# Kernel tuning notes

Measured on AMD Instinct MI355X. Metric: run time of the kernel, lower is better.

The kernel has to match this reference:

```python
import jax, jax.numpy as jnp
import numpy as np

N = 50000      # nodes per graph batch (per siamese side)
E = 500000     # edges per side
F_IN = 128     # input_channels
H = 128        # hidden_channels
OUT = 2        # output_channels
G = 512        # number of graphs in the batch


def setup_inputs() -> dict:
    key = jax.random.key(0)
    ks = jax.random.split(key, 16)

    def lin_w(k, fan_in, shape):
        lim = 1.0 / np.sqrt(fan_in)
        return jax.random.uniform(k, shape, jnp.float32, -lim, lim)

    return {
        "x1": jax.random.normal(ks[0], (N, F_IN), jnp.float32),
        "x2": jax.random.normal(ks[1], (N, F_IN), jnp.float32),
        "edge_index1": jax.random.randint(ks[2], (2, E), 0, N, jnp.int32),
        "edge_index2": jax.random.randint(ks[3], (2, E), 0, N, jnp.int32),
        "batch1": jnp.sort(jax.random.randint(ks[4], (N,), 0, G, jnp.int32)),
        "batch2": jnp.sort(jax.random.randint(ks[5], (N,), 0, G, jnp.int32)),
        "W1": lin_w(ks[6], F_IN, (F_IN, H)), "b1": jnp.zeros((H,), jnp.float32),
        "W2": lin_w(ks[7], H, (H, H)),       "b2": jnp.zeros((H,), jnp.float32),
        "W3": lin_w(ks[8], H, (H, H)),       "b3": jnp.zeros((H,), jnp.float32),
        "Wc1": lin_w(ks[9], 2 * H, (2 * H, 4 * H)), "bc1": jnp.zeros((4 * H,), jnp.float32),
        "Wc2": lin_w(ks[10], 4 * H, (4 * H, 2 * H)), "bc2": jnp.zeros((2 * H,), jnp.float32),
        "Wc3": lin_w(ks[11], 2 * H, (2 * H, OUT)),   "bc3": jnp.zeros((OUT,), jnp.float32),
        "num_graphs": G,
    }


def _gcn_layer(x, W, b, src, dst, dinv):
    # PyG GCNConv: linear transform, then deg^{-1/2} A_hat deg^{-1/2} aggregation + bias
    h = x @ W
    msg = h[src] * (dinv[src] * dinv[dst])[:, None]   # [E+N, H]
    return jax.ops.segment_sum(msg, dst, num_segments=x.shape[0]) + b


def _forward_once(x, edge_index, batch, W1, b1, W2, b2, W3, b3, num_graphs):
    n = x.shape[0]
    loop = jnp.arange(n, dtype=edge_index.dtype)
    src = jnp.concatenate([edge_index[0], loop])      # add self-loops
    dst = jnp.concatenate([edge_index[1], loop])
    deg = jax.ops.segment_sum(jnp.ones_like(dst, dtype=x.dtype), dst, num_segments=n)
    dinv = jax.lax.rsqrt(deg)                          # deg >= 1 due to self-loops
    h = jax.nn.relu(_gcn_layer(x, W1, b1, src, dst, dinv))
    h = jax.nn.relu(_gcn_layer(h, W2, b2, src, dst, dinv))
    h = _gcn_layer(h, W3, b3, src, dst, dinv)
    # global_mean_pool over batch indices
    s = jax.ops.segment_sum(h, batch, num_segments=num_graphs)
    cnt = jax.ops.segment_sum(jnp.ones((n,), x.dtype), batch, num_segments=num_graphs)
    return s / jnp.maximum(cnt, 1.0)[:, None]


def reference(x1, x2, edge_index1, edge_index2, batch1, batch2,
              W1, b1, W2, b2, W3, b3, Wc1, bc1, Wc2, bc2, Wc3, bc3, num_graphs):
    g1 = _forward_once(x1, edge_index1, batch1, W1, b1, W2, b2, W3, b3, num_graphs)
    g2 = _forward_once(x2, edge_index2, batch2, W1, b1, W2, b2, W3, b3, num_graphs)
    z = jnp.concatenate([g1, g2], axis=1)             # [G, 2H]
    z = jax.nn.relu(z @ Wc1 + bc1)
    z = jax.nn.relu(z @ Wc2 + bc2)
    # dropout p=0.5 is identity at eval time
    return z @ Wc3 + bc3                               # [G, OUT]
```

## Files before the change

### kernel.cpp

```cpp
#include <hip/hip_runtime.h>
#include <math.h>

#define N_NODES 50000
#define E_EDGES 500000
#define HDIM    128
#define OUTC    2
#define NGRAPH  512

typedef _Float16 f16x8 __attribute__((ext_vector_type(8)));
typedef float    f32x4 __attribute__((ext_vector_type(4)));

__global__ void k_zero(int* __restrict__ p, int n) {
    int i = blockIdx.x * blockDim.x + threadIdx.x;
    int stride = gridDim.x * blockDim.x;
    for (; i < n; i += stride) p[i] = 0;
}

__global__ void k_hist(const int* __restrict__ d0, const int* __restrict__ d1,
                       int ecnt, int off1, int* __restrict__ cnt) {
    int i = blockIdx.x * blockDim.x + threadIdx.x;
    int stride = gridDim.x * blockDim.x;
    for (; i < ecnt; i += stride) {
        int d = (i < E_EDGES) ? d0[i] : d1[i - E_EDGES] + off1;
        atomicAdd(&cnt[d], 1);
    }
}

__global__ void k_scan_a(const int* __restrict__ cnt, int* __restrict__ excl,
                         int* __restrict__ blksum, float* __restrict__ dinv,
                         const int* __restrict__ bt0, const int* __restrict__ bt1,
                         int goff0, int nn, int nside, float* __restrict__ cnt_g) {
    __shared__ int s[512];
    int t = threadIdx.x;
    int i = blockIdx.x * 512 + t;
    int v = 0;
    if (i < nn) {
        v = cnt[i];
        dinv[i] = 1.0f / sqrtf((float)(v + 1));
        int g = (i < nside) ? bt0[i] + goff0 : bt1[i - nside] + NGRAPH;
        atomicAdd(&cnt_g[g], 1.0f);
    }
    s[t] = v; __syncthreads();
    for (int off = 1; off < 512; off <<= 1) {
        int add = (t >= off) ? s[t - off] : 0;
        __syncthreads();
        s[t] += add;
        __syncthreads();
    }
    if (i < nn) excl[i] = s[t] - v;
    if (t == 511) blksum[blockIdx.x] = s[511];
}

__global__ void k_scan_b(int* __restrict__ blksum, int nb) {
    __shared__ int s[512];
    int t = threadIdx.x;
    int v = (t < nb) ? blksum[t] : 0;
    s[t] = v; __syncthreads();
    for (int off = 1; off < 512; off <<= 1) {
        int add = (t >= off) ? s[t - off] : 0;
        __syncthreads();
        s[t] += add;
        __syncthreads();
    }
    if (t < nb) blksum[t] = s[t] - v;
}

__global__ void k_scan_c(int* __restrict__ excl, const int* __restrict__ blksum,
                         int nn, int tot) {
    int t = threadIdx.x;
    int i = blockIdx.x * 512 + t;
    if (i < nn) excl[i] += blksum[blockIdx.x];
    if (i == 0) excl[nn] = tot;
}

__global__ void k_fill(const int* __restrict__ s0, const int* __restrict__ s1,
                       const int* __restrict__ d0, const int* __restrict__ d1,
                       int ecnt, int off1,
                       const int* __restrict__ row_ptr, int* __restrict__ fill_cnt,
                       const float* __restrict__ dinv, int2* __restrict__ edges) {
    int i = blockIdx.x * blockDim.x + threadIdx.x;
    int stride = gridDim.x * blockDim.x;
    for (; i < ecnt; i += stride) {
        int d, sg;
        if (i < E_EDGES) { sg = s0[i]; d = d0[i]; }
        else             { sg = s1[i - E_EDGES] + off1; d = d1[i - E_EDGES] + off1; }
        int p = atomicAdd(&fill_cnt[d], 1);
        float w = dinv[sg] * dinv[d];
        edges[row_ptr[d] + p] = make_int2(sg, __float_as_int(w));
    }
}

__global__ void k_cvt(const float* __restrict__ x0, const float* __restrict__ x1,
                      int nside_pairs, int total_pairs,
                      _Float16* __restrict__ hi, _Float16* __restrict__ lo) {
    int i = blockIdx.x * blockDim.x + threadIdx.x;
    int stride = gridDim.x * blockDim.x;
    for (; i < total_pairs; i += stride) {
        float2 v = (i < nside_pairs) ? ((const float2*)x0)[i]
                                     : ((const float2*)x1)[i - nside_pairs];
        _Float16 hx = (_Float16)v.x, hy = (_Float16)v.y;
        _Float16 lx = (_Float16)(v.x - (float)hx), ly = (_Float16)(v.y - (float)hy);
        union { _Float16 h[2]; unsigned u; } ph, pl;
        ph.h[0] = hx; ph.h[1] = hy;
        pl.h[0] = lx; pl.h[1] = ly;
        ((unsigned*)hi)[i] = ph.u;
        ((unsigned*)lo)[i] = pl.u;
    }
}

__global__ void k_cvtw(const float* __restrict__ W,
                       _Float16* __restrict__ thi, _Float16* __restrict__ tlo) {
    int i = blockIdx.x * blockDim.x + threadIdx.x;
    if (i >= 128 * 128) return;
    int n = i >> 7, k = i & 127;
    float v = W[k * 128 + n];
    _Float16 h = (_Float16)v;
    thi[i] = h;
    tlo[i] = (_Float16)(v - (float)h);
}

__global__ __launch_bounds__(256) void k_gemm_splitf16(
        const _Float16* __restrict__ Ahi, const _Float16* __restrict__ Alo,
        const _Float16* __restrict__ Bhi, const _Float16* __restrict__ Blo,
        float* __restrict__ C, int M) {
    __shared__ _Float16 sA[2][128][40];
    __shared__ _Float16 sB[2][128][40];
    int tid = threadIdx.x;
    int wave = tid >> 6, lane = tid & 63;
    int wm = (wave >> 1) * 64;
    int wn = (wave & 1) * 64;
    int quad = lane >> 4, fm = lane & 15;
    int row0 = blockIdx.x * 128;

    int lr = tid >> 2;
    int lk = (tid & 3) * 8;

    f32x4 acc[4][4] = {};

    const float4 z4 = make_float4(0.f, 0.f, 0.f, 0.f);
    for (int kc = 0; kc < 128; kc += 32) {
        int r1 = row0 + lr, r2 = row0 + lr + 64;
        bool ok1 = r1 < M, ok2 = r2 < M;
        float4 ah1 = ok1 ? *(const float4*)(Ahi + (size_t)r1 * 128 + kc + lk) : z4;
        float4 al1 = ok1 ? *(const float4*)(Alo + (size_t)r1 * 128 + kc + lk) : z4;
        float4 ah2 = ok2 ? *(const float4*)(Ahi + (size_t)r2 * 128 + kc + lk) : z4;
        float4 al2 = ok2 ? *(const float4*)(Alo + (size_t)r2 * 128 + kc + lk) : z4;
        float4 bh1 = *(const float4*)(Bhi + (size_t)lr * 128 + kc + lk);
        float4 bl1 = *(const float4*)(Blo + (size_t)lr * 128 + kc + lk);
        float4 bh2 = *(const float4*)(Bhi + (size_t)(lr + 64) * 128 + kc + lk);
        float4 bl2 = *(const float4*)(Blo + (size_t)(lr + 64) * 128 + kc + lk);
        __syncthreads();
        *(float4*)&sA[0][lr][lk]      = ah1;
        *(float4*)&sA[1][lr][lk]      = al1;
        *(float4*)&sA[0][lr + 64][lk] = ah2;
        *(float4*)&sA[1][lr + 64][lk] = al2;
        *(float4*)&sB[0][lr][lk]      = bh1;
        *(float4*)&sB[1][lr][lk]      = bl1;
        *(float4*)&sB[0][lr + 64][lk] = bh2;
        *(float4*)&sB[1][lr + 64][lk] = bl2;
        __syncthreads();

        f16x8 afh[4], afl[4], bfh[4], bfl[4];
#pragma unroll
        for (int mi = 0; mi < 4; mi++) {
            afh[mi] = *(const f16x8*)&sA[0][wm + mi * 16 + fm][quad * 8];
            afl[mi] = *(const f16x8*)&sA[1][wm + mi * 16 + fm][quad * 8];
        }
#pragma unroll
        for (int ni = 0; ni < 4; ni++) {
            bfh[ni] = *(const f16x8*)&sB[0][wn + ni * 16 + fm][quad * 8];
            bfl[ni] = *(const f16x8*)&sB[1][wn + ni * 16 + fm][quad * 8];
        }
#pragma unroll
        for (int mi = 0; mi < 4; mi++)
#pragma unroll
            for (int ni = 0; ni < 4; ni++) {
                acc[mi][ni] = __builtin_amdgcn_mfma_f32_16x16x32_f16(afh[mi], bfh[ni], acc[mi][ni], 0, 0, 0);
                acc[mi][ni] = __builtin_amdgcn_mfma_f32_16x16x32_f16(afh[mi], bfl[ni], acc[mi][ni], 0, 0, 0);
                acc[mi][ni] = __builtin_amdgcn_mfma_f32_16x16x32_f16(afl[mi], bfh[ni], acc[mi][ni], 0, 0, 0);
            }
    }

#pragma unroll
    for (int mi = 0; mi < 4; mi++)
#pragma unroll
        for (int reg = 0; reg < 4; reg++) {
            int r = row0 + wm + mi * 16 + quad * 4 + reg;
            if (r >= M) continue;
#pragma unroll
            for (int ni = 0; ni < 4; ni++)
                C[(size_t)r * 128 + wn + ni * 16 + fm] = acc[mi][ni][reg];
        }
}

__global__ __launch_bounds__(256) void k_gemm(
        const float* __restrict__ A, const float* __restrict__ B,
        const float* __restrict__ bias, float* __restrict__ C,
        int M, int Nn, int K, int ldc, int act) {
    __shared__ float As[16][64];
    __shared__ float Bs[16][68];
    int tid = threadIdx.x;
    int tx = tid & 15, ty = tid >> 4;
    int row0 = blockIdx.x * 64, col0 = blockIdx.y * 64;
    float acc[4][4] = {};
    int arow = tid >> 2;
    int acol = (tid & 3) * 4;
    int brow = tid >> 4;
    int bcol = (tid & 15) * 4;

    for (int k0 = 0; k0 < K; k0 += 16) {
        float4 av = make_float4(0.f, 0.f, 0.f, 0.f);
        int ar = row0 + arow;
        if (ar < M) av = *(const float4*)(A + (size_t)ar * K + k0 + acol);
        As[acol + 0][arow] = av.x;
        As[acol + 1][arow] = av.y;
        As[acol + 2][arow] = av.z;
        As[acol + 3][arow] = av.w;

        float4 bv = make_float4(0.f, 0.f, 0.f, 0.f);
        const float* Brow = B + (size_t)(k0 + brow) * Nn;
        int bc = col0 + bcol;
        if (bc + 3 < Nn) {
            bv = *(const float4*)(Brow + bc);
        } else {
            if (bc     < Nn) bv.x = Brow[bc];
            if (bc + 1 < Nn) bv.y = Brow[bc + 1];
            if (bc + 2 < Nn) bv.z = Brow[bc + 2];
        }
        Bs[brow][bcol + 0] = bv.x;
        Bs[brow][bcol + 1] = bv.y;
        Bs[brow][bcol + 2] = bv.z;
        Bs[brow][bcol + 3] = bv.w;
        __syncthreads();

#pragma unroll
        for (int k = 0; k < 16; k++) {
            float4 a = *(const float4*)&As[k][ty * 4];
            float4 b = *(const float4*)&Bs[k][tx * 4];
            acc[0][0] += a.x * b.x; acc[0][1] += a.x * b.y; acc[0][2] += a.x * b.z; acc[0][3] += a.x * b.w;
            acc[1][0] += a.y * b.x; acc[1][1] += a.y * b.y; acc[1][2] += a.y * b.z; acc[1][3] += a.y * b.w;
            acc[2][0] += a.z * b.x; acc[2][1] += a.z * b.y; acc[2][2] += a.z * b.z; acc[2][3] += a.z * b.w;
            acc[3][0] += a.w * b.x; acc[3][1] += a.w * b.y; acc[3][2] += a.w * b.z; acc[3][3] += a.w * b.w;
        }
        __syncthreads();
    }

#pragma unroll
    for (int i = 0; i < 4; i++) {
        int r = row0 + ty * 4 + i;
        if (r >= M) continue;
#pragma unroll
        for (int j = 0; j < 4; j++) {
            int c = col0 + tx * 4 + j;
            if (c >= Nn) continue;
            float v = acc[i][j];
            if (bias) v += bias[c];
            if (act) v = fmaxf(v, 0.0f);
            C[(size_t)r * ldc + c] = v;
        }
    }
}

template <int MODE, int PACK>
__global__ __launch_bounds__(256) void k_agg(
        const float* __restrict__ H, const float* __restrict__ dinv,
        const int* __restrict__ row_ptr, const int2* __restrict__ edges,
        const float* __restrict__ bias,
        _Float16* __restrict__ outHi, _Float16* __restrict__ outLo,
        float* __restrict__ outF,
        const int* __restrict__ bt0, const int* __restrict__ bt1,
        int goff0, int nnodes, int nside, float* __restrict__ pool) {
    int wave = threadIdx.x >> 6, lane = threadIdx.x & 63;
    int node = blockIdx.x * 4 + wave;
    if (node >= nnodes) return;

    float di = dinv[node];
    float2 hv = ((const float2*)(H + (size_t)node * HDIM))[lane];
    float wself = di * di;
    float ax = hv.x * wself;
    float ay = hv.y * wself;

    int rs = __builtin_amdgcn_readfirstlane(row_ptr[node]);
    int re = __builtin_amdgcn_readfirstlane(row_ptr[node + 1]);
    for (int base = rs; base < re; base += 8) {
        int nrem = re - base;
        int m = nrem - 1;
        int i1 = 1 < nrem ? 1 : m;
        int i2 = 2 < nrem ? 2 : m;
        int i3 = 3 < nrem ? 3 : m;
        int i4 = 4 < nrem ? 4 : m;
        int i5 = 5 < nrem ? 5 : m;
        int i6 = 6 < nrem ? 6 : m;
        int i7 = 7 < nrem ? 7 : m;
        int2 E0 = edges[base];
        int2 E1 = edges[base + i1];
        int2 E2 = edges[base + i2];
        int2 E3 = edges[base + i3];
        int2 E4 = edges[base + i4];
        int2 E5 = edges[base + i5];
        int2 E6 = edges[base + i6];
        int2 E7 = edges[base + i7];
        float2 v0 = ((const float2*)(H + (size_t)E0.x * HDIM))[lane];
        float2 v1 = ((const float2*)(H + (size_t)E1.x * HDIM))[lane];
        float2 v2 = ((const float2*)(H + (size_t)E2.x * HDIM))[lane];
        float2 v3 = ((const float2*)(H + (size_t)E3.x * HDIM))[lane];
        float2 v4 = ((const float2*)(H + (size_t)E4.x * HDIM))[lane];
        float2 v5 = ((const float2*)(H + (size_t)E5.x * HDIM))[lane];
        float2 v6 = ((const float2*)(H + (size_t)E6.x * HDIM))[lane];
        float2 v7 = ((const float2*)(H + (size_t)E7.x * HDIM))[lane];
        float w0 = __int_as_float(E0.y);
        float w1 = 1 < nrem ? __int_as_float(E1.y) : 0.f;
        float w2 = 2 < nrem ? __int_as_float(E2.y) : 0.f;
        float w3 = 3 < nrem ? __int_as_float(E3.y) : 0.f;
        float w4 = 4 < nrem ? __int_as_float(E4.y) : 0.f;
        float w5 = 5 < nrem ? __int_as_float(E5.y) : 0.f;
        float w6 = 6 < nrem ? __int_as_float(E6.y) : 0.f;
        float w7 = 7 < nrem ? __int_as_float(E7.y) : 0.f;
        ax = fmaf(v0.x, w0, ax); ay = fmaf(v0.y, w0, ay);
        ax = fmaf(v1.x, w1, ax); ay = fmaf(v1.y, w1, ay);
        ax = fmaf(v2.x, w2, ax); ay = fmaf(v2.y, w2, ay);
        ax = fmaf(v3.x, w3, ax); ay = fmaf(v3.y, w3, ay);
        ax = fmaf(v4.x, w4, ax); ay = fmaf(v4.y, w4, ay);
        ax = fmaf(v5.x, w5, ax); ay = fmaf(v5.y, w5, ay);
        ax = fmaf(v6.x, w6, ax); ay = fmaf(v6.y, w6, ay);
        ax = fmaf(v7.x, w7, ax); ay = fmaf(v7.y, w7, ay);
    }

    if (MODE == 2) {
        int g = (node < nside) ? bt0[node] + goff0 : bt1[node - nside] + NGRAPH;
        float* p = pool + (size_t)g * HDIM + lane * 2;
        atomicAdd(p,     ax);
        atomicAdd(p + 1, ay);
    } else {
        float ox = fmaxf(ax + bias[lane * 2],     0.0f);
        float oy = fmaxf(ay + bias[lane * 2 + 1], 0.0f);
        if (PACK) {
            _Float16 hx = (_Float16)ox, hy = (_Float16)oy;
            _Float16 lx = (_Float16)(ox - (float)hx), ly = (_Float16)(oy - (float)hy);
            union { _Float16 h[2]; unsigned u; } ph, pl;
            ph.h[0] = hx; ph.h[1] = hy;
            pl.h[0] = lx; pl.h[1] = ly;
            ((unsigned*)(outHi + (size_t)node * HDIM))[lane] = ph.u;
            ((unsigned*)(outLo + (size_t)node * HDIM))[lane] = pl.u;
        } else {
            ((float2*)(outF + (size_t)node * HDIM))[lane] = make_float2(ox, oy);
        }
    }
}

__global__ void k_divpool(float* __restrict__ pool, const float* __restrict__ cnt_g) {
    int i = blockIdx.x * blockDim.x + threadIdx.x;
    if (i < 2 * NGRAPH * HDIM) pool[i] /= fmaxf(cnt_g[i >> 7], 1.0f);
}

extern "C" void kernel_launch(void* const* d_in, const int* in_sizes, int n_in,
                              void* d_out, int out_size, void* d_ws, size_t ws_size,
                              hipStream_t stream) {
    (void)in_sizes; (void)n_in; (void)out_size;

    const float* x[2]  = {(const float*)d_in[0], (const float*)d_in[1]};
    const int*   ei[2] = {(const int*)d_in[2], (const int*)d_in[3]};
    const int*   bt[2] = {(const int*)d_in[4], (const int*)d_in[5]};
    const float* W1  = (const float*)d_in[6];  const float* b1  = (const float*)d_in[7];
    const float* W2  = (const float*)d_in[8];  const float* b2  = (const float*)d_in[9];
    const float* W3  = (const float*)d_in[10]; const float* b3  = (const float*)d_in[11];
    const float* Wc1 = (const float*)d_in[12]; const float* bc1 = (const float*)d_in[13];
    const float* Wc2 = (const float*)d_in[14]; const float* bc2 = (const float*)d_in[15];
    const float* Wc3 = (const float*)d_in[16]; const float* bc3 = (const float*)d_in[17];
    float* out = (float*)d_out;

    const bool batched = ws_size >= 120ull * 1000 * 1000;
    const int NN = batched ? 2 * N_NODES : N_NODES;
    const int NE = batched ? 2 * E_EDGES : E_EDGES;

    char* ws = (char*)d_ws;
    size_t off = 0;
    auto carve = [&](size_t bytes) -> char* {
        char* p = ws + off;
        off += (bytes + 255) & ~(size_t)255;
        return p;
    };

    int*   edge_cnt = (int*)  carve((size_t)NN * 4);
    int*   fill_cnt = (int*)  carve((size_t)NN * 4);
    float* pool_s   = (float*)carve((size_t)2 * NGRAPH * HDIM * 4);
    float* cnt_g    = (float*)carve((size_t)2 * NGRAPH * 4);
    float* dinv     = (float*)carve((size_t)NN * 4);
    int*   row_ptr  = (int*)  carve((size_t)(NN + 1) * 4);
    int2*  edges    = (int2*) carve((size_t)NE * 8);
    int*   blksum   = (int*)  carve(1024 * 4);
    _Float16* wt    = (_Float16*)carve(4 * 128 * 128 * 2);
    _Float16* hS    = (_Float16*)carve((size_t)NN * HDIM * 4);
    float* hA       = (float*)carve((size_t)NN * HDIM * 4);
    float* zcat     = (float*)carve((size_t)NGRAPH * 2 * HDIM * 4);
    float* z1       = (float*)carve((size_t)NGRAPH * 4 * HDIM * 4);
    float* z2       = (float*)carve((size_t)NGRAPH * 2 * HDIM * 4);

    _Float16* w1hi = wt;
    _Float16* w1lo = wt + 128 * 128;
    _Float16* w2hi = wt + 2 * 128 * 128;
    _Float16* w2lo = wt + 3 * 128 * 128;
    _Float16* hShi = hS;
    _Float16* hSlo = hS + (size_t)NN * HDIM;
    float*    hSf  = (float*)hS;

    int zeroA_words = (int)(((char*)pool_s - (char*)edge_cnt) / 4);
    int zeroB_words = (int)(((char*)dinv   - (char*)pool_s)   / 4);

    k_zero<<<256, 256, 0, stream>>>((int*)pool_s, zeroB_words);
    k_cvtw<<<64, 256, 0, stream>>>(W1, w1hi, w1lo);
    k_cvtw<<<64, 256, 0, stream>>>(W2, w2hi, w2lo);

    const int gblk = (NN + 127) / 128;

    if (batched) {
        const int nscan = (2 * N_NODES + 511) / 512;
        const int ablk  = (2 * N_NODES + 3) / 4;

        k_zero<<<512, 256, 0, stream>>>(edge_cnt, zeroA_words);
        k_hist<<<1024, 256, 0, stream>>>(ei[0] + E_EDGES, ei[1] + E_EDGES,
                                         2 * E_EDGES, N_NODES, edge_cnt);
        k_scan_a<<<nscan, 512, 0, stream>>>(edge_cnt, row_ptr, blksum, dinv,
                                            bt[0], bt[1], 0, 2 * N_NODES, N_NODES, cnt_g);
        k_scan_b<<<1, 512, 0, stream>>>(blksum, nscan);
        k_scan_c<<<nscan, 512, 0, stream>>>(row_ptr, blksum, 2 * N_NODES, 2 * E_EDGES);
        k_fill<<<1024, 256, 0, stream>>>(ei[0], ei[1], ei[0] + E_EDGES, ei[1] + E_EDGES,
                                         2 * E_EDGES, N_NODES, row_ptr, fill_cnt, dinv, edges);

        k_cvt<<<1024, 256, 0, stream>>>(x[0], x[1], N_NODES * HDIM / 2,
                                        2 * N_NODES * HDIM / 2, hShi, hSlo);

        k_gemm_splitf16<<<gblk, 256, 0, stream>>>(hShi, hSlo, w1hi, w1lo, hA, 2 * N_NODES);
        k_agg<0, 1><<<ablk, 256, 0, stream>>>(hA, dinv, row_ptr, edges, b1,
                                              hShi, hSlo, nullptr, bt[0], bt[1], 0,
                                              2 * N_NODES, N_NODES, nullptr);
        k_gemm_splitf16<<<gblk, 256, 0, stream>>>(hShi, hSlo, w2hi, w2lo, hA, 2 * N_NODES);
        k_agg<0, 0><<<ablk, 256, 0, stream>>>(hA, dinv, row_ptr, edges, b2,
                                              nullptr, nullptr, hSf, bt[0], bt[1], 0,
                                              2 * N_NODES, N_NODES, nullptr);
        k_agg<2, 0><<<ablk, 256, 0, stream>>>(hSf, dinv, row_ptr, edges, nullptr,
                                              nullptr, nullptr, nullptr, bt[0], bt[1], 0,
                                              2 * N_NODES, N_NODES, pool_s);
    } else {
        const int nscan = (N_NODES + 511) / 512;
        const int ablk  = (N_NODES + 3) / 4;

        for (int s = 0; s < 2; ++s) {
            const int* esrc = ei[s];
            const int* edst = ei[s] + E_EDGES;
            int goff = s * NGRAPH;

            k_zero<<<512, 256, 0, stream>>>(edge_cnt, zeroA_words);
            k_hist<<<512, 256, 0, stream>>>(edst, edst, E_EDGES, 0, edge_cnt);
            k_scan_a<<<nscan, 512, 0, stream>>>(edge_cnt, row_ptr, blksum, dinv,
                                                bt[s], bt[s], goff, N_NODES, N_NODES, cnt_g);
            k_scan_b<<<1, 512, 0, stream>>>(blksum, nscan);
            k_scan_c<<<nscan, 512, 0, stream>>>(row_ptr, blksum, N_NODES, E_EDGES);
            k_fill<<<512, 256, 0, stream>>>(esrc, esrc, edst, edst, E_EDGES, 0,
                                            row_ptr, fill_cnt, dinv, edges);

            k_cvt<<<1024, 256, 0, stream>>>(x[s], x[s], N_NODES * HDIM / 2,
                                            N_NODES * HDIM / 2, hShi, hSlo);

            k_gemm_splitf16<<<gblk, 256, 0, stream>>>(hShi, hSlo, w1hi, w1lo, hA, N_NODES);
            k_agg<0, 1><<<ablk, 256, 0, stream>>>(hA, dinv, row_ptr, edges, b1,
                                                  hShi, hSlo, nullptr, bt[s], bt[s], goff,
                                                  N_NODES, N_NODES, nullptr);
            k_gemm_splitf16<<<gblk, 256, 0, stream>>>(hShi, hSlo, w2hi, w2lo, hA, N_NODES);
            k_agg<0, 0><<<ablk, 256, 0, stream>>>(hA, dinv, row_ptr, edges, b2,
                                                  nullptr, nullptr, hSf, bt[s], bt[s], goff,
                                                  N_NODES, N_NODES, nullptr);
            k_agg<2, 0><<<ablk, 256, 0, stream>>>(hSf, dinv, row_ptr, edges, nullptr,
                                                  nullptr, nullptr, nullptr, bt[s], bt[s], goff,
                                                  N_NODES, N_NODES, pool_s);
        }
    }

    k_divpool<<<(2 * NGRAPH * HDIM + 255) / 256, 256, 0, stream>>>(pool_s, cnt_g);

    for (int s = 0; s < 2; ++s)
        k_gemm<<<dim3(NGRAPH / 64, HDIM / 64), 256, 0, stream>>>(
            pool_s + (size_t)s * NGRAPH * HDIM, W3, b3, zcat + s * HDIM,
            NGRAPH, HDIM, HDIM, 2 * HDIM, 0);

    k_gemm<<<dim3(NGRAPH / 64, (4 * HDIM) / 64), 256, 0, stream>>>(zcat, Wc1, bc1, z1, NGRAPH, 4 * HDIM, 2 * HDIM, 4 * HDIM, 1);
    k_gemm<<<dim3(NGRAPH / 64, (2 * HDIM) / 64), 256, 0, stream>>>(z1, Wc2, bc2, z2, NGRAPH, 2 * HDIM, 4 * HDIM, 2 * HDIM, 1);
    k_gemm<<<dim3(NGRAPH / 64, 1), 256, 0, stream>>>(z2, Wc3, bc3, out, NGRAPH, OUTC, 2 * HDIM, OUTC, 0);
}
```

Before: 704.7 us.

## Fuse input conversion into GEMM, merge prep kernels, prefetch edges in aggregation

Removes the separate fp32-to-split-fp16 conversion pass over the node features by converting inside the first GEMM's tile load. Merges the zeroing and weight conversion kernels into one prep launch. Folds the mean-pool division into a single pooled W3 GEMM that handles both sides. Software-prefetches the next batch of edge records in the aggregation loop, which raises register use in exchange for overlapping edge loads with feature gathers.

```diff
diff --git a/kernel.cpp b/kernel.cpp
--- a/kernel.cpp
+++ b/kernel.cpp
@@ -10,10 +10,23 @@
 typedef _Float16 f16x8 __attribute__((ext_vector_type(8)));
 typedef float    f32x4 __attribute__((ext_vector_type(4)));
 
-__global__ void k_zero(int* __restrict__ p, int n) {
+__global__ void k_prep(int* __restrict__ zA, int nA, int* __restrict__ zB, int nB,
+                       const float* __restrict__ W1, const float* __restrict__ W2,
+                       _Float16* __restrict__ w1hi, _Float16* __restrict__ w1lo,
+                       _Float16* __restrict__ w2hi, _Float16* __restrict__ w2lo) {
     int i = blockIdx.x * blockDim.x + threadIdx.x;
     int stride = gridDim.x * blockDim.x;
-    for (; i < n; i += stride) p[i] = 0;
+    for (int j = i; j < nA; j += stride) zA[j] = 0;
+    for (int j = i; j < nB; j += stride) zB[j] = 0;
+    for (int j = i; j < 128 * 128; j += stride) {
+        int n = j >> 7, k = j & 127;
+        float v = W1[k * 128 + n];
+        _Float16 h = (_Float16)v;
+        w1hi[j] = h; w1lo[j] = (_Float16)(v - (float)h);
+        v = W2[k * 128 + n];
+        h = (_Float16)v;
+        w2hi[j] = h; w2lo[j] = (_Float16)(v - (float)h);
+    }
 }
 
 __global__ void k_hist(const int* __restrict__ d0, const int* __restrict__ d1,
@@ -90,36 +103,19 @@
     }
 }
 
-__global__ void k_cvt(const float* __restrict__ x0, const float* __restrict__ x1,
-                      int nside_pairs, int total_pairs,
-                      _Float16* __restrict__ hi, _Float16* __restrict__ lo) {
-    int i = blockIdx.x * blockDim.x + threadIdx.x;
-    int stride = gridDim.x * blockDim.x;
-    for (; i < total_pairs; i += stride) {
-        float2 v = (i < nside_pairs) ? ((const float2*)x0)[i]
-                                     : ((const float2*)x1)[i - nside_pairs];
-        _Float16 hx = (_Float16)v.x, hy = (_Float16)v.y;
-        _Float16 lx = (_Float16)(v.x - (float)hx), ly = (_Float16)(v.y - (float)hy);
-        union { _Float16 h[2]; unsigned u; } ph, pl;
-        ph.h[0] = hx; ph.h[1] = hy;
-        pl.h[0] = lx; pl.h[1] = ly;
-        ((unsigned*)hi)[i] = ph.u;
-        ((unsigned*)lo)[i] = pl.u;
-    }
-}
-
-__global__ void k_cvtw(const float* __restrict__ W,
-                       _Float16* __restrict__ thi, _Float16* __restrict__ tlo) {
-    int i = blockIdx.x * blockDim.x + threadIdx.x;
-    if (i >= 128 * 128) return;
-    int n = i >> 7, k = i & 127;
-    float v = W[k * 128 + n];
-    _Float16 h = (_Float16)v;
-    thi[i] = h;
-    tlo[i] = (_Float16)(v - (float)h);
-}
-
-__global__ __launch_bounds__(256) void k_gemm_splitf16(
+__device__ inline void cvt8(const float4& p, const float4& q, f16x8& h, f16x8& l) {
+    float v[8] = {p.x, p.y, p.z, p.w, q.x, q.y, q.z, q.w};
+#pragma unroll
+    for (int i = 0; i < 8; i++) {
+        _Float16 hh = (_Float16)v[i];
+        h[i] = hh;
+        l[i] = (_Float16)(v[i] - (float)hh);
+    }
+}
+
+template <int ASRC>
+__global__ __launch_bounds__(256) void k_gemm_split(
+        const float* __restrict__ A0f, const float* __restrict__ A1f, int nside,
         const _Float16* __restrict__ Ahi, const _Float16* __restrict__ Alo,
         const _Float16* __restrict__ Bhi, const _Float16* __restrict__ Blo,
         float* __restrict__ C, int M) {
@@ -136,28 +132,43 @@
     int lk = (tid & 3) * 8;
 
     f32x4 acc[4][4] = {};
-
     const float4 z4 = make_float4(0.f, 0.f, 0.f, 0.f);
+
     for (int kc = 0; kc < 128; kc += 32) {
         int r1 = row0 + lr, r2 = row0 + lr + 64;
         bool ok1 = r1 < M, ok2 = r2 < M;
-        float4 ah1 = ok1 ? *(const float4*)(Ahi + (size_t)r1 * 128 + kc + lk) : z4;
-        float4 al1 = ok1 ? *(const float4*)(Alo + (size_t)r1 * 128 + kc + lk) : z4;
-        float4 ah2 = ok2 ? *(const float4*)(Ahi + (size_t)r2 * 128 + kc + lk) : z4;
-        float4 al2 = ok2 ? *(const float4*)(Alo + (size_t)r2 * 128 + kc + lk) : z4;
-        float4 bh1 = *(const float4*)(Bhi + (size_t)lr * 128 + kc + lk);
-        float4 bl1 = *(const float4*)(Blo + (size_t)lr * 128 + kc + lk);
-        float4 bh2 = *(const float4*)(Bhi + (size_t)(lr + 64) * 128 + kc + lk);
-        float4 bl2 = *(const float4*)(Blo + (size_t)(lr + 64) * 128 + kc + lk);
-        __syncthreads();
-        *(float4*)&sA[0][lr][lk]      = ah1;
-        *(float4*)&sA[1][lr][lk]      = al1;
-        *(float4*)&sA[0][lr + 64][lk] = ah2;
-        *(float4*)&sA[1][lr + 64][lk] = al2;
-        *(float4*)&sB[0][lr][lk]      = bh1;
-        *(float4*)&sB[1][lr][lk]      = bl1;
-        *(float4*)&sB[0][lr + 64][lk] = bh2;
-        *(float4*)&sB[1][lr + 64][lk] = bl2;
+        f16x8 ah1, al1, ah2, al2;
+        if (ASRC == 1) {
+            const float* p1 = (r1 < nside) ? A0f + (size_t)r1 * 128
+                                           : A1f + (size_t)(r1 - nside) * 128;
+            const float* p2 = (r2 < nside) ? A0f + (size_t)r2 * 128
+                                           : A1f + (size_t)(r2 - nside) * 128;
+            float4 a = ok1 ? *(const float4*)(p1 + kc + lk) : z4;
+            float4 b = ok1 ? *(const float4*)(p1 + kc + lk + 4) : z4;
+            float4 c = ok2 ? *(const float4*)(p2 + kc + lk) : z4;
+            float4 d = ok2 ? *(const float4*)(p2 + kc + lk + 4) : z4;
+            cvt8(a, b, ah1, al1);
+            cvt8(c, d, ah2, al2);
+        } else {
+            const f16x8 zf = {};
+            ah1 = ok1 ? *(const f16x8*)(Ahi + (size_t)r1 * 128 + kc + lk) : zf;
+            al1 = ok1 ? *(const f16x8*)(Alo + (size_t)r1 * 128 + kc + lk) : zf;
+            ah2 = ok2 ? *(const f16x8*)(Ahi + (size_t)r2 * 128 + kc + lk) : zf;
+            al2 = ok2 ? *(const f16x8*)(Alo + (size_t)r2 * 128 + kc + lk) : zf;
+        }
+        f16x8 bh1 = *(const f16x8*)(Bhi + (size_t)lr * 128 + kc + lk);
+        f16x8 bl1 = *(const f16x8*)(Blo + (size_t)lr * 128 + kc + lk);
+        f16x8 bh2 = *(const f16x8*)(Bhi + (size_t)(lr + 64) * 128 + kc + lk);
+        f16x8 bl2 = *(const f16x8*)(Blo + (size_t)(lr + 64) * 128 + kc + lk);
+        __syncthreads();
+        *(f16x8*)&sA[0][lr][lk]      = ah1;
+        *(f16x8*)&sA[1][lr][lk]      = al1;
+        *(f16x8*)&sA[0][lr + 64][lk] = ah2;
+        *(f16x8*)&sA[1][lr + 64][lk] = al2;
+        *(f16x8*)&sB[0][lr][lk]      = bh1;
+        *(f16x8*)&sB[1][lr][lk]      = bl1;
+        *(f16x8*)&sB[0][lr + 64][lk] = bh2;
+        *(f16x8*)&sB[1][lr + 64][lk] = bl2;
         __syncthreads();
 
         f16x8 afh[4], afl[4], bfh[4], bfl[4];
@@ -261,6 +272,63 @@
     }
 }
 
+__global__ __launch_bounds__(256) void k_gemm_pool(
+        const float* __restrict__ pool, const float* __restrict__ cnt_g,
+        const float* __restrict__ W, const float* __restrict__ bias,
+        float* __restrict__ zcat) {
+    __shared__ float As[16][64];
+    __shared__ float Bs[16][68];
+    int side = blockIdx.z;
+    const float* A = pool + (size_t)side * NGRAPH * HDIM;
+    const float* cg = cnt_g + side * NGRAPH;
+    int tid = threadIdx.x;
+    int tx = tid & 15, ty = tid >> 4;
+    int row0 = blockIdx.x * 64, col0 = blockIdx.y * 64;
+    float acc[4][4] = {};
+    int arow = tid >> 2;
+    int acol = (tid & 3) * 4;
+    int brow = tid >> 4;
+    int bcol = (tid & 15) * 4;
+
+    for (int k0 = 0; k0 < 128; k0 += 16) {
+        int ar = row0 + arow;
+        float sc = 1.0f / fmaxf(cg[ar], 1.0f);
+        float4 av = *(const float4*)(A + (size_t)ar * 128 + k0 + acol);
+        As[acol + 0][arow] = av.x * sc;
+        As[acol + 1][arow] = av.y * sc;
+        As[acol + 2][arow] = av.z * sc;
+        As[acol + 3][arow] = av.w * sc;
+
+        float4 bv = *(const float4*)(W + (size_t)(k0 + brow) * 128 + col0 + bcol);
+        Bs[brow][bcol + 0] = bv.x;
+        Bs[brow][bcol + 1] = bv.y;
+        Bs[brow][bcol + 2] = bv.z;
+        Bs[brow][bcol + 3] = bv.w;
+        __syncthreads();
+
+#pragma unroll
+        for (int k = 0; k < 16; k++) {
+            float4 a = *(const float4*)&As[k][ty * 4];
+            float4 b = *(const float4*)&Bs[k][tx * 4];
+            acc[0][0] += a.x * b.x; acc[0][1] += a.x * b.y; acc[0][2] += a.x * b.z; acc[0][3] += a.x * b.w;
+            acc[1][0] += a.y * b.x; acc[1][1] += a.y * b.y; acc[1][2] += a.y * b.z; acc[1][3] += a.y * b.w;
+            acc[2][0] += a.z * b.x; acc[2][1] += a.z * b.y; acc[2][2] += a.z * b.z; acc[2][3] += a.z * b.w;
+            acc[3][0] += a.w * b.x; acc[3][1] += a.w * b.y; acc[3][2] += a.w * b.z; acc[3][3] += a.w * b.w;
+        }
+        __syncthreads();
+    }
+
+#pragma unroll
+    for (int i = 0; i < 4; i++) {
+        int r = row0 + ty * 4 + i;
+#pragma unroll
+        for (int j = 0; j < 4; j++) {
+            int c = col0 + tx * 4 + j;
+            zcat[(size_t)r * 256 + side * 128 + c] = acc[i][j] + bias[c];
+        }
+    }
+}
+
 template <int MODE, int PACK>
 __global__ __launch_bounds__(256) void k_agg(
         const float* __restrict__ H, const float* __restrict__ dinv,
@@ -282,24 +350,35 @@
 
     int rs = __builtin_amdgcn_readfirstlane(row_ptr[node]);
     int re = __builtin_amdgcn_readfirstlane(row_ptr[node + 1]);
+
+    int2 E0, E1, E2, E3, E4, E5, E6, E7;
+    if (rs < re) {
+        int nrem = re - rs, m = nrem - 1;
+        E0 = edges[rs];
+        E1 = edges[rs + (1 < nrem ? 1 : m)];
+        E2 = edges[rs + (2 < nrem ? 2 : m)];
+        E3 = edges[rs + (3 < nrem ? 3 : m)];
+        E4 = edges[rs + (4 < nrem ? 4 : m)];
+        E5 = edges[rs + (5 < nrem ? 5 : m)];
+        E6 = edges[rs + (6 < nrem ? 6 : m)];
+        E7 = edges[rs + (7 < nrem ? 7 : m)];
+    }
+
     for (int base = rs; base < re; base += 8) {
-        int nrem = re - base;
-        int m = nrem - 1;
-        int i1 = 1 < nrem ? 1 : m;
-        int i2 = 2 < nrem ? 2 : m;
-        int i3 = 3 < nrem ? 3 : m;
-        int i4 = 4 < nrem ? 4 : m;
-        int i5 = 5 < nrem ? 5 : m;
-        int i6 = 6 < nrem ? 6 : m;
-        int i7 = 7 < nrem ? 7 : m;
-        int2 E0 = edges[base];
-        int2 E1 = edges[base + i1];
-        int2 E2 = edges[base + i2];
-        int2 E3 = edges[base + i3];
-        int2 E4 = edges[base + i4];
-        int2 E5 = edges[base + i5];
-        int2 E6 = edges[base + i6];
-        int2 E7 = edges[base + i7];
+        int nb = base + 8;
+        int2 P0 = E0, P1 = E1, P2 = E2, P3 = E3, P4 = E4, P5 = E5, P6 = E6, P7 = E7;
+        if (nb < re) {
+            int nr2 = re - nb, m2 = nr2 - 1;
+            P0 = edges[nb];
+            P1 = edges[nb + (1 < nr2 ? 1 : m2)];
+            P2 = edges[nb + (2 < nr2 ? 2 : m2)];
+            P3 = edges[nb + (3 < nr2 ? 3 : m2)];
+            P4 = edges[nb + (4 < nr2 ? 4 : m2)];
+            P5 = edges[nb + (5 < nr2 ? 5 : m2)];
+            P6 = edges[nb + (6 < nr2 ? 6 : m2)];
+            P7 = edges[nb + (7 < nr2 ? 7 : m2)];
+        }
+
         float2 v0 = ((const float2*)(H + (size_t)E0.x * HDIM))[lane];
         float2 v1 = ((const float2*)(H + (size_t)E1.x * HDIM))[lane];
         float2 v2 = ((const float2*)(H + (size_t)E2.x * HDIM))[lane];
@@ -308,6 +387,8 @@
         float2 v5 = ((const float2*)(H + (size_t)E5.x * HDIM))[lane];
         float2 v6 = ((const float2*)(H + (size_t)E6.x * HDIM))[lane];
         float2 v7 = ((const float2*)(H + (size_t)E7.x * HDIM))[lane];
+
+        int nrem = re - base;
         float w0 = __int_as_float(E0.y);
         float w1 = 1 < nrem ? __int_as_float(E1.y) : 0.f;
         float w2 = 2 < nrem ? __int_as_float(E2.y) : 0.f;
@@ -316,6 +397,7 @@
         float w5 = 5 < nrem ? __int_as_float(E5.y) : 0.f;
         float w6 = 6 < nrem ? __int_as_float(E6.y) : 0.f;
         float w7 = 7 < nrem ? __int_as_float(E7.y) : 0.f;
+
         ax = fmaf(v0.x, w0, ax); ay = fmaf(v0.y, w0, ay);
         ax = fmaf(v1.x, w1, ax); ay = fmaf(v1.y, w1, ay);
         ax = fmaf(v2.x, w2, ax); ay = fmaf(v2.y, w2, ay);
@@ -324,6 +406,9 @@
         ax = fmaf(v5.x, w5, ax); ay = fmaf(v5.y, w5, ay);
         ax = fmaf(v6.x, w6, ax); ay = fmaf(v6.y, w6, ay);
         ax = fmaf(v7.x, w7, ax); ay = fmaf(v7.y, w7, ay);
+
+        E0 = P0; E1 = P1; E2 = P2; E3 = P3;
+        E4 = P4; E5 = P5; E6 = P6; E7 = P7;
     }
 
     if (MODE == 2) {
@@ -348,11 +433,6 @@
     }
 }
 
-__global__ void k_divpool(float* __restrict__ pool, const float* __restrict__ cnt_g) {
-    int i = blockIdx.x * blockDim.x + threadIdx.x;
-    if (i < 2 * NGRAPH * HDIM) pool[i] /= fmaxf(cnt_g[i >> 7], 1.0f);
-}
-
 extern "C" void kernel_launch(void* const* d_in, const int* in_sizes, int n_in,
                               void* d_out, int out_size, void* d_ws, size_t ws_size,
                               hipStream_t stream) {
@@ -407,17 +487,14 @@
     int zeroA_words = (int)(((char*)pool_s - (char*)edge_cnt) / 4);
     int zeroB_words = (int)(((char*)dinv   - (char*)pool_s)   / 4);
 
-    k_zero<<<256, 256, 0, stream>>>((int*)pool_s, zeroB_words);
-    k_cvtw<<<64, 256, 0, stream>>>(W1, w1hi, w1lo);
-    k_cvtw<<<64, 256, 0, stream>>>(W2, w2hi, w2lo);
-
     const int gblk = (NN + 127) / 128;
 
     if (batched) {
         const int nscan = (2 * N_NODES + 511) / 512;
         const int ablk  = (2 * N_NODES + 3) / 4;
 
-        k_zero<<<512, 256, 0, stream>>>(edge_cnt, zeroA_words);
+        k_prep<<<512, 256, 0, stream>>>(edge_cnt, zeroA_words, (int*)pool_s, zeroB_words,
+                                        W1, W2, w1hi, w1lo, w2hi, w2lo);
         k_hist<<<1024, 256, 0, stream>>>(ei[0] + E_EDGES, ei[1] + E_EDGES,
                                          2 * E_EDGES, N_NODES, edge_cnt);
         k_scan_a<<<nscan, 512, 0, stream>>>(edge_cnt, row_ptr, blksum, dinv,
@@ -427,14 +504,13 @@
         k_fill<<<1024, 256, 0, stream>>>(ei[0], ei[1], ei[0] + E_EDGES, ei[1] + E_EDGES,
                                          2 * E_EDGES, N_NODES, row_ptr, fill_cnt, dinv, edges);
 
-        k_cvt<<<1024, 256, 0, stream>>>(x[0], x[1], N_NODES * HDIM / 2,
-                                        2 * N_NODES * HDIM / 2, hShi, hSlo);
-
-        k_gemm_splitf16<<<gblk, 256, 0, stream>>>(hShi, hSlo, w1hi, w1lo, hA, 2 * N_NODES);
+        k_gemm_split<1><<<gblk, 256, 0, stream>>>(x[0], x[1], N_NODES,
+                                                  nullptr, nullptr, w1hi, w1lo, hA, 2 * N_NODES);
         k_agg<0, 1><<<ablk, 256, 0, stream>>>(hA, dinv, row_ptr, edges, b1,
                                               hShi, hSlo, nullptr, bt[0], bt[1], 0,
                                               2 * N_NODES, N_NODES, nullptr);
-        k_gemm_splitf16<<<gblk, 256, 0, stream>>>(hShi, hSlo, w2hi, w2lo, hA, 2 * N_NODES);
+        k_gemm_split<0><<<gblk, 256, 0, stream>>>(nullptr, nullptr, 0,
+                                                  hShi, hSlo, w2hi, w2lo, hA, 2 * N_NODES);
         k_agg<0, 0><<<ablk, 256, 0, stream>>>(hA, dinv, row_ptr, edges, b2,
                                               nullptr, nullptr, hSf, bt[0], bt[1], 0,
                                               2 * N_NODES, N_NODES, nullptr);
@@ -445,12 +521,16 @@
         const int nscan = (N_NODES + 511) / 512;
         const int ablk  = (N_NODES + 3) / 4;
 
+        k_prep<<<512, 256, 0, stream>>>(edge_cnt, zeroA_words, (int*)pool_s, zeroB_words,
+                                        W1, W2, w1hi, w1lo, w2hi, w2lo);
         for (int s = 0; s < 2; ++s) {
             const int* esrc = ei[s];
             const int* edst = ei[s] + E_EDGES;
             int goff = s * NGRAPH;
 
-            k_zero<<<512, 256, 0, stream>>>(edge_cnt, zeroA_words);
+            if (s == 1)
+                k_prep<<<512, 256, 0, stream>>>(edge_cnt, zeroA_words, (int*)pool_s, 0,
+                                                W1, W2, w1hi, w1lo, w2hi, w2lo);
             k_hist<<<512, 256, 0, stream>>>(edst, edst, E_EDGES, 0, edge_cnt);
             k_scan_a<<<nscan, 512, 0, stream>>>(edge_cnt, row_ptr, blksum, dinv,
                                                 bt[s], bt[s], goff, N_NODES, N_NODES, cnt_g);
@@ -459,14 +539,13 @@
             k_fill<<<512, 256, 0, stream>>>(esrc, esrc, edst, edst, E_EDGES, 0,
                                             row_ptr, fill_cnt, dinv, edges);
 
-            k_cvt<<<1024, 256, 0, stream>>>(x[s], x[s], N_NODES * HDIM / 2,
-                                            N_NODES * HDIM / 2, hShi, hSlo);
-
-            k_gemm_splitf16<<<gblk, 256, 0, stream>>>(hShi, hSlo, w1hi, w1lo, hA, N_NODES);
+            k_gemm_split<1><<<gblk, 256, 0, stream>>>(x[s], x[s], N_NODES,
+                                                      nullptr, nullptr, w1hi, w1lo, hA, N_NODES);
             k_agg<0, 1><<<ablk, 256, 0, stream>>>(hA, dinv, row_ptr, edges, b1,
                                                   hShi, hSlo, nullptr, bt[s], bt[s], goff,
                                                   N_NODES, N_NODES, nullptr);
-            k_gemm_splitf16<<<gblk, 256, 0, stream>>>(hShi, hSlo, w2hi, w2lo, hA, N_NODES);
+            k_gemm_split<0><<<gblk, 256, 0, stream>>>(nullptr, nullptr, 0,
+                                                      hShi, hSlo, w2hi, w2lo, hA, N_NODES);
             k_agg<0, 0><<<ablk, 256, 0, stream>>>(hA, dinv, row_ptr, edges, b2,
                                                   nullptr, nullptr, hSf, bt[s], bt[s], goff,
                                                   N_NODES, N_NODES, nullptr);
@@ -476,12 +555,7 @@
         }
     }
 
-    k_divpool<<<(2 * NGRAPH * HDIM + 255) / 256, 256, 0, stream>>>(pool_s, cnt_g);
-
-    for (int s = 0; s < 2; ++s)
-        k_gemm<<<dim3(NGRAPH / 64, HDIM / 64), 256, 0, stream>>>(
-            pool_s + (size_t)s * NGRAPH * HDIM, W3, b3, zcat + s * HDIM,
-            NGRAPH, HDIM, HDIM, 2 * HDIM, 0);
+    k_gemm_pool<<<dim3(NGRAPH / 64, 2, 2), 256, 0, stream>>>(pool_s, cnt_g, W3, b3, zcat);
 
     k_gemm<<<dim3(NGRAPH / 64, (4 * HDIM) / 64), 256, 0, stream>>>(zcat, Wc1, bc1, z1, NGRAPH, 4 * HDIM, 2 * HDIM, 4 * HDIM, 1);
     k_gemm<<<dim3(NGRAPH / 64, (2 * HDIM) / 64), 256, 0, stream>>>(z1, Wc2, bc2, z2, NGRAPH, 2 * HDIM, 4 * HDIM, 2 * HDIM, 1);
```

New measurement: 676.6 us. -4.0%, faster.
